# Kernel tuning notes

Hardware: AMD Instinct MI355X
Metric: run time of the kernel (lower is better)

Reference implementation:

```python
import jax, jax.numpy as jnp
import numpy as np

jax.config.update("jax_enable_x64", True)  # torch code casts to double for the logdet

B, N = 64, 512
MIN_LEN = 384  # variable sentence lengths to exercise padding path


def _matrix_tree_logZ(s_arc, mask):
    """log partition of non-projective trees via Kirchhoff's Matrix-Tree theorem.

    s_arc: [B, n, n] float32 scores of (dependent i, head j) pairs.
    mask:  [B, n] bool, column 0 is the root pseudo-word (False on input).
    """
    n = s_arc.shape[-1]
    m = mask.at[:, 0].set(True)                      # index_fill(1, 0, 1)
    chart = m[:, :, None] & m[:, None, :]            # [B, n, n]
    s = jnp.where(chart, s_arc, -jnp.inf)            # masked_fill(~chart, -inf)
    A = jnp.exp(s).astype(jnp.float64)               # exp(-inf) = 0 on padding
    d = A.sum(-1)                                    # D diagonal: row sums [B, n]
    eye = jnp.eye(n, dtype=A.dtype)
    L_full = d[:, :, None] * eye - A                 # D - A (Laplacian)
    # rows of padding tokens are identity rows (masked_scatter_ onto eye)
    L = jnp.where(m[:, :, None], L_full, eye[None])
    # logdet of the minor removing root row/col
    _, logabsdet = jnp.linalg.slogdet(L[:, 1:, 1:])
    return logabsdet.sum().astype(jnp.float32)


def setup_inputs() -> dict:
    key = jax.random.key(0)
    k1, k2, k3 = jax.random.split(key, 3)
    scores = jax.random.normal(k1, (B, N, N), dtype=jnp.float32)
    lens = jax.random.randint(k2, (B,), MIN_LEN, N)
    pos = jnp.arange(N)
    # first column False (root pseudo-word), True for real tokens < length
    mask = (pos[None, :] < lens[:, None]) & (pos[None, :] > 0)
    target = jax.random.randint(k3, (B, N), 0, N)    # gold head indices
    return {"scores": scores, "mask": mask, "target": target}


def reference(scores, mask, target):
    # forward(scores, mask, target, mbr=True, partial=False)
    logZ, marginals = jax.value_and_grad(_matrix_tree_logZ)(scores, mask)
    gold = jnp.take_along_axis(scores, target[..., None], axis=-1).squeeze(-1)  # [B, N]
    gold_score = jnp.where(mask, gold, 0.0).sum()    # scores[mask].sum()
    loss = (logZ - gold_score) / mask.sum()
    return loss, marginals
```

## Files before the change

kernel.cpp:

```cpp
#include <hip/hip_runtime.h>
#include <math.h>

#define BATCH 64
#define NN 512
#define MS 511
#define LDM 512
#define MSTRIDE ((size_t)MS*LDM)
#define OSTRIDE ((size_t)NN*NN)
#define PB 64
#define YW(r,c) (((r)<<5) + ((((c) + ((((r)>>3)&7)<<2))) & 31))

__global__ void k_convert(const void* __restrict__ mask_raw,
                          const void* __restrict__ tgt_raw,
                          int* __restrict__ cmask, int* __restrict__ ctgt) {
  int b = blockIdx.x;
  const unsigned char* mb = (const unsigned char*)mask_raw;
  const int* mw = (const int*)mask_raw;
  const int* tw = (const int*)tgt_raw;
  bool m_bytes = (mb[1] | mb[2] | mb[3]) != 0;
  bool m_64 = false;
  if (!m_bytes) {
    int acc = 0;
    for (int j = 1; j < 32; j += 2) acc |= mw[j];
    m_64 = (acc == 0);
  }
  int tacc = 0;
  for (int j = 1; j < 32; j += 2) tacc |= tw[j];
  bool t_64 = (tacc == 0);
  for (int i = threadIdx.x; i < NN; i += blockDim.x) {
    size_t idx = (size_t)b * NN + i;
    int mv;
    if (m_bytes) mv = mb[idx] != 0;
    else if (m_64) mv = mw[2 * idx] != 0;
    else mv = mw[idx] != 0;
    cmask[idx] = mv;
    ctgt[idx] = t_64 ? tw[2 * idx] : tw[idx];
  }
}

__global__ void k_build_M(const float* __restrict__ scores,
                          const int* __restrict__ mask,
                          float* __restrict__ M) {
  int b = blockIdx.y;
  int ip = blockIdx.x;
  int i = ip + 1;
  const int* mrow = mask + (size_t)b * NN;
  float* Mrow = M + (size_t)b * MSTRIDE + (size_t)ip * LDM;
  int tid = threadIdx.x;
  if (!mrow[i]) {
    for (int jp = tid; jp < MS; jp += 256)
      Mrow[jp] = (jp == ip) ? 1.0f : 0.0f;
    if (tid == 0) Mrow[MS] = 0.0f;
    return;
  }
  const float* srow = scores + ((size_t)b * NN + i) * NN;
  double part = 0.0;
  for (int j = tid; j < NN; j += 256) {
    bool mj = (j == 0) || (mrow[j] != 0);
    float e = mj ? expf(srow[j]) : 0.0f;
    part += (double)e;
    if (j >= 1) Mrow[j - 1] = -e;
  }
  __shared__ double red[256];
  red[tid] = part;
  __syncthreads();
  for (int s = 128; s > 0; s >>= 1) {
    if (tid < s) red[tid] += red[tid + s];
    __syncthreads();
  }
  if (tid == (i & 255)) Mrow[ip] += (float)red[0];
  if (tid == 0) Mrow[MS] = 0.0f;
}

__global__ __launch_bounds__(512) void k_panel64(float* __restrict__ M, int kb,
                                                 double* __restrict__ ld2) {
  int b = blockIdx.x;
  float* Mb = M + (size_t)b * MSTRIDE;
  int tid = threadIdx.x;
  __shared__ float A[64 * 65];
  __shared__ float XU[64 * 66];
  __shared__ float XL[64 * 66];
  __shared__ double lg[64];

  for (int idx = tid; idx < 64 * 64; idx += 512) {
    int r = idx >> 6, c = idx & 63;
    int gr = kb + r, gc = kb + c;
    A[r * 65 + c] = (gr < MS && gc < MS) ? Mb[(size_t)gr * LDM + gc]
                                         : ((r == c) ? 1.0f : 0.0f);
  }
  __syncthreads();

  int rr = tid >> 3, sub = tid & 7;
  for (int j = 0; j < 63; ++j) {
    if (rr > j) {
      float piv = A[j * 65 + j];
      float l = A[rr * 65 + j] / piv;
      if (sub == 0) A[rr * 65 + j] = l;
      for (int c = j + 1 + sub; c < 64; c += 8)
        A[rr * 65 + c] -= l * A[j * 65 + c];
    }
    __syncthreads();
  }
  if (tid < 64) lg[tid] = log(fabs((double)A[tid * 65 + tid]));
  __syncthreads();
  if (tid == 0) {
    double a = 0.0;
    for (int j = 0; j < 64; ++j) a += lg[j];
    ld2[(kb >> 6) * BATCH + b] = a;
  }

  {
    int c = rr;
    if (sub == 0) XU[c * 66 + c] = 1.0f / A[c * 65 + c];
    for (int r2 = c - 1; r2 >= 0; --r2) {
      float s = 0.0f;
      for (int k = r2 + 1 + sub; k <= c; k += 8)
        s += A[r2 * 65 + k] * XU[c * 66 + k];
      s += __shfl_xor(s, 1, 8);
      s += __shfl_xor(s, 2, 8);
      s += __shfl_xor(s, 4, 8);
      if (sub == 0) XU[c * 66 + r2] = -s / A[r2 * 65 + r2];
    }
  }
  {
    int c = rr;
    if (sub == 0) XL[c * 66 + c] = 1.0f;
    for (int r2 = c + 1; r2 < 64; ++r2) {
      float s = 0.0f;
      for (int k = c + sub; k < r2; k += 8)
        s += A[r2 * 65 + k] * XL[c * 66 + k];
      s += __shfl_xor(s, 1, 8);
      s += __shfl_xor(s, 2, 8);
      s += __shfl_xor(s, 4, 8);
      if (sub == 0) XL[c * 66 + r2] = -s;
    }
  }
  __syncthreads();
  for (int idx = tid; idx < 4096; idx += 512) {
    int r = idx >> 6, c = idx & 63;
    int gr = kb + r, gc = kb + c;
    if (gr < MS && gc < MS)
      Mb[(size_t)gr * LDM + gc] = (r > c) ? XL[c * 66 + r] : XU[c * 66 + r];
  }
}

__global__ __launch_bounds__(256) void k_trsm(float* __restrict__ M, int kb) {
  int b = blockIdx.z;
  int t = blockIdx.x;
  int side = blockIdx.y;
  float* Mb = M + (size_t)b * MSTRIDE;
  __shared__ float Fs[64 * 65];
  __shared__ float As[64 * 65];
  int tid = threadIdx.x;
  int off = kb + 64 + t * 64;
  for (int idx = tid; idx < 4096; idx += 256) {
    int r = idx >> 6, c = idx & 63;
    int gr = kb + r, gc = kb + c;
    float v;
    if (gr < MS && gc < MS) {
      float d = Mb[(size_t)gr * LDM + gc];
      if (side == 0) v = (r > c) ? d : (r == c ? 1.0f : 0.0f);
      else           v = (r <= c) ? d : 0.0f;
    } else {
      v = (r == c) ? 1.0f : 0.0f;
    }
    Fs[r * 65 + c] = v;
  }
  for (int idx = tid; idx < 4096; idx += 256) {
    int r = idx >> 6, c = idx & 63;
    int gr, gc;
    if (side == 0) { gr = kb + r; gc = off + c; }
    else           { gr = off + r; gc = kb + c; }
    As[r * 65 + c] = (gr < MS && gc < MS) ? Mb[(size_t)gr * LDM + gc] : 0.0f;
  }
  __syncthreads();
  int tx = tid & 15, ty = tid >> 4;
  float acc[4][4];
#pragma unroll
  for (int i = 0; i < 4; ++i)
#pragma unroll
    for (int j = 0; j < 4; ++j) acc[i][j] = 0.0f;
  if (side == 0) {
#pragma unroll 4
    for (int k = 0; k < 64; ++k) {
      float av[4], bv[4];
#pragma unroll
      for (int i = 0; i < 4; ++i) av[i] = Fs[(ty * 4 + i) * 65 + k];
#pragma unroll
      for (int j = 0; j < 4; ++j) bv[j] = As[k * 65 + tx * 4 + j];
#pragma unroll
      for (int i = 0; i < 4; ++i)
#pragma unroll
        for (int j = 0; j < 4; ++j) acc[i][j] = fmaf(av[i], bv[j], acc[i][j]);
    }
  } else {
#pragma unroll 4
    for (int k = 0; k < 64; ++k) {
      float av[4], bv[4];
#pragma unroll
      for (int i = 0; i < 4; ++i) av[i] = As[(ty * 4 + i) * 65 + k];
#pragma unroll
      for (int j = 0; j < 4; ++j) bv[j] = Fs[k * 65 + tx * 4 + j];
#pragma unroll
      for (int i = 0; i < 4; ++i)
#pragma unroll
        for (int j = 0; j < 4; ++j) acc[i][j] = fmaf(av[i], bv[j], acc[i][j]);
    }
  }
  if (side == 0) {
    int gc = off + tx * 4;
    if (gc < MS) {
#pragma unroll
      for (int i = 0; i < 4; ++i) {
        int gr = kb + ty * 4 + i;
        *(float4*)&Mb[(size_t)gr * LDM + gc] =
            make_float4(acc[i][0], acc[i][1], acc[i][2], acc[i][3]);
      }
    }
  } else {
#pragma unroll
    for (int i = 0; i < 4; ++i) {
      int gr = off + ty * 4 + i;
      if (gr < MS)
        *(float4*)&Mb[(size_t)gr * LDM + kb + tx * 4] =
            make_float4(acc[i][0], acc[i][1], acc[i][2], acc[i][3]);
    }
  }
}

__global__ __launch_bounds__(256) void k_update_panel(float* __restrict__ M, int kb,
                                                      double* __restrict__ ld2) {
  int b = blockIdx.z;
  float* Mb = M + (size_t)b * MSTRIDE;
  int row0 = kb + PB + blockIdx.x * 128;
  int col0 = kb + PB + blockIdx.y * 128;
  __shared__ __align__(16) float smem[128 * 68 + 64 * 132];
  __shared__ double lg[64];
  float* As = smem;
  float* Bs = smem + 128 * 68;
  int tid = threadIdx.x;
  for (int idx = tid; idx < 2048; idx += 256) {
    int r = idx >> 4, q = (idx & 15) * 4;
    int gr = row0 + r;
    float4 v = make_float4(0.f, 0.f, 0.f, 0.f);
    if (gr < MS) v = *(const float4*)&Mb[(size_t)gr * LDM + kb + q];
    *(float4*)&As[r * 68 + q] = v;
  }
  for (int idx = tid; idx < 2048; idx += 256) {
    int r = idx >> 5, q = (idx & 31) * 4;
    int gc = col0 + q;
    float4 v = make_float4(0.f, 0.f, 0.f, 0.f);
    if (gc < MS)
      v = *(const float4*)&Mb[(size_t)(kb + r) * LDM + gc];
    *(float4*)&Bs[r * 132 + q] = v;
  }
  __syncthreads();
  int tx = tid & 15, ty = tid >> 4;
  int gc0 = col0 + tx * 4, gc1 = gc0 + 64;
  bool c0v = gc0 < MS, c1v = gc1 < MS;
  float4 acc[8][2];
#pragma unroll
  for (int i = 0; i < 8; ++i) {
    int gr = row0 + ty + 16 * i;
    bool rv = gr < MS;
    acc[i][0] = (rv && c0v) ? *(const float4*)&Mb[(size_t)gr * LDM + gc0]
                            : make_float4(0.f, 0.f, 0.f, 0.f);
    acc[i][1] = (rv && c1v) ? *(const float4*)&Mb[(size_t)gr * LDM + gc1]
                            : make_float4(0.f, 0.f, 0.f, 0.f);
  }
#pragma unroll 2
  for (int k = 0; k < 64; ++k) {
    float4 b0 = *(const float4*)&Bs[k * 132 + tx * 4];
    float4 b1 = *(const float4*)&Bs[k * 132 + tx * 4 + 64];
    float av[8];
#pragma unroll
    for (int i = 0; i < 8; ++i) av[i] = As[(ty + 16 * i) * 68 + k];
#pragma unroll
    for (int i = 0; i < 8; ++i) {
      float a = av[i];
      acc[i][0].x = fmaf(-a, b0.x, acc[i][0].x);
      acc[i][0].y = fmaf(-a, b0.y, acc[i][0].y);
      acc[i][0].z = fmaf(-a, b0.z, acc[i][0].z);
      acc[i][0].w = fmaf(-a, b0.w, acc[i][0].w);
      acc[i][1].x = fmaf(-a, b1.x, acc[i][1].x);
      acc[i][1].y = fmaf(-a, b1.y, acc[i][1].y);
      acc[i][1].z = fmaf(-a, b1.z, acc[i][1].z);
      acc[i][1].w = fmaf(-a, b1.w, acc[i][1].w);
    }
  }
#pragma unroll
  for (int i = 0; i < 8; ++i) {
    int gr = row0 + ty + 16 * i;
    if (gr < MS) {
      if (c0v) *(float4*)&Mb[(size_t)gr * LDM + gc0] = acc[i][0];
      if (c1v) *(float4*)&Mb[(size_t)gr * LDM + gc1] = acc[i][1];
    }
  }

  if (blockIdx.x == 0 && blockIdx.y == 0) {
    int kbn = kb + PB;
    float* A2 = smem;
    float* XU = smem + 4160;
    float* XL = smem + 4160 + 4224;
    __syncthreads();
    for (int idx = tid; idx < 4096; idx += 256) {
      int r = idx >> 6, c = idx & 63;
      int gr = kbn + r, gc = kbn + c;
      A2[r * 65 + c] = (gr < MS && gc < MS) ? Mb[(size_t)gr * LDM + gc]
                                            : ((r == c) ? 1.0f : 0.0f);
    }
    __syncthreads();
    int rr = tid >> 2, sub = tid & 3;
    for (int j = 0; j < 63; ++j) {
      if (rr > j) {
        float piv = A2[j * 65 + j];
        float l = A2[rr * 65 + j] / piv;
        if (sub == 0) A2[rr * 65 + j] = l;
        for (int c = j + 1 + sub; c < 64; c += 4)
          A2[rr * 65 + c] -= l * A2[j * 65 + c];
      }
      __syncthreads();
    }
    if (tid < 64) lg[tid] = log(fabs((double)A2[tid * 65 + tid]));
    __syncthreads();
    if (tid == 0) {
      double a = 0.0;
      for (int j = 0; j < 64; ++j) a += lg[j];
      ld2[(kbn >> 6) * BATCH + b] = a;
    }
    {
      int c = rr;
      if (sub == 0) XU[c * 66 + c] = 1.0f / A2[c * 65 + c];
      for (int r2 = c - 1; r2 >= 0; --r2) {
        float s = 0.0f;
        for (int k = r2 + 1 + sub; k <= c; k += 4)
          s += A2[r2 * 65 + k] * XU[c * 66 + k];
        s += __shfl_xor(s, 1, 4);
        s += __shfl_xor(s, 2, 4);
        if (sub == 0) XU[c * 66 + r2] = -s / A2[r2 * 65 + r2];
      }
    }
    {
      int c = rr;
      if (sub == 0) XL[c * 66 + c] = 1.0f;
      for (int r2 = c + 1; r2 < 64; ++r2) {
        float s = 0.0f;
        for (int k = c + sub; k < r2; k += 4)
          s += A2[r2 * 65 + k] * XL[c * 66 + k];
        s += __shfl_xor(s, 1, 4);
        s += __shfl_xor(s, 2, 4);
        if (sub == 0) XL[c * 66 + r2] = -s;
      }
    }
    __syncthreads();
    for (int idx = tid; idx < 4096; idx += 256) {
      int r = idx >> 6, c = idx & 63;
      int gr = kbn + r, gc = kbn + c;
      if (gr < MS && gc < MS)
        Mb[(size_t)gr * LDM + gc] = (r > c) ? XL[c * 66 + r] : XU[c * 66 + r];
    }
  }
}

__device__ __forceinline__ void diag_pass(const float* __restrict__ Mb,
                                          float* __restrict__ Yt,
                                          int jb, int tid, int UPPER) {
  int drg = tid >> 3, dcg = tid & 7;
  int dr = jb + drg;
  bool vr = dr < MS;
  const float* Pr = Mb + (size_t)dr * LDM + jb;
  float4 da = make_float4(0.f, 0.f, 0.f, 0.f);
#pragma unroll 4
  for (int q = 0; q < 16; ++q) {
    float4 t = vr ? *(const float4*)&Pr[4 * q] : make_float4(0.f, 0.f, 0.f, 0.f);
#pragma unroll
    for (int m = 0; m < 4; ++m) {
      int cc = 4 * q + m;
      float tm = (m == 0) ? t.x : ((m == 1) ? t.y : ((m == 2) ? t.z : t.w));
      float a;
      if (UPPER) a = (drg <= cc) ? tm : 0.0f;
      else       a = (drg > cc) ? tm : ((drg == cc) ? 1.0f : 0.0f);
      float4 bv = *(const float4*)&Yt[YW(jb + cc, 4 * dcg)];
      da.x = fmaf(a, bv.x, da.x); da.y = fmaf(a, bv.y, da.y);
      da.z = fmaf(a, bv.z, da.z); da.w = fmaf(a, bv.w, da.w);
    }
  }
  __syncthreads();
  *(float4*)&Yt[YW(jb + drg, 4 * dcg)] = da;
  __syncthreads();
}

__device__ __forceinline__ void offdiag_pass(const float* __restrict__ Mb,
                                             float* __restrict__ Yt,
                                             int jb, int rowBase, int nr,
                                             int tid, int cg, int rg) {
  if (nr <= 0) return;
  int row0 = rowBase + 8 * rg;
  int nv = nr - 8 * rg;
  if (nv <= 0) return;
  nv = nv > 8 ? 8 : nv;
  float4 a0[8];
#pragma unroll
  for (int i = 0; i < 8; ++i)
    a0[i] = (i < nv) ? *(const float4*)&Yt[YW(row0 + i, 4 * cg)]
                     : make_float4(0.f, 0.f, 0.f, 0.f);
  const float* Ar = Mb + (size_t)row0 * LDM + jb;
#pragma unroll 2
  for (int kh = 0; kh < 16; ++kh) {
    float4 pA[8];
#pragma unroll
    for (int i = 0; i < 8; ++i)
      pA[i] = (i < nv) ? *(const float4*)&Ar[(size_t)i * LDM + 4 * kh]
                       : make_float4(0.f, 0.f, 0.f, 0.f);
    __builtin_amdgcn_s_setprio(1);
#pragma unroll
    for (int k = 0; k < 4; ++k) {
      float4 bv = *(const float4*)&Yt[YW(jb + 4 * kh + k, 4 * cg)];
#define AK(i) ((k == 0) ? pA[i].x : ((k == 1) ? pA[i].y : ((k == 2) ? pA[i].z : pA[i].w)))
#define RF(i) { \
      float av_ = AK(i); \
      a0[i].x = fmaf(-av_, bv.x, a0[i].x); a0[i].y = fmaf(-av_, bv.y, a0[i].y); \
      a0[i].z = fmaf(-av_, bv.z, a0[i].z); a0[i].w = fmaf(-av_, bv.w, a0[i].w); }
      RF(0) RF(1) RF(2) RF(3) RF(4) RF(5) RF(6) RF(7)
#undef RF
#undef AK
    }
    __builtin_amdgcn_s_setprio(0);
  }
#pragma unroll
  for (int i = 0; i < 8; ++i) {
    if (i < nv)
      *(float4*)&Yt[YW(row0 + i, 4 * cg)] = a0[i];
  }
}

__global__ __launch_bounds__(512, 4) void k_solve(const float* __restrict__ M,
                                                  const float* __restrict__ scores,
                                                  const int* __restrict__ mask,
                                                  float* __restrict__ out1) {
  int id = blockIdx.x;
  int xcd = id & 7, k7 = id >> 3;
  int b = xcd + ((k7 >> 4) << 3);
  int cb = k7 & 15;
  const float* Mb = M + (size_t)b * MSTRIDE;
  int tid = threadIdx.x;
  int c0 = cb * 32, fb = c0 & ~63;
  __shared__ __align__(16) float Yt[512 * 32];
  int cg = tid & 7, rg = tid >> 3;

  for (int idx = tid; idx < 4096; idx += 512)
    ((float4*)Yt)[idx] = make_float4(0.f, 0.f, 0.f, 0.f);
  __syncthreads();
  {
    int coff = c0 - fb;
    int r2 = tid >> 3, q4 = (tid & 7) << 2;
    int gr = fb + r2;
    int c_ = coff + q4;
    float e0, e1, e2, e3;
    if (gr < MS) {
      float4 d = *(const float4*)&Mb[(size_t)gr * LDM + fb + c_];
      e0 = (r2 > c_) ? d.x : ((r2 == c_) ? 1.f : 0.f);
      e1 = (r2 > c_ + 1) ? d.y : ((r2 == c_ + 1) ? 1.f : 0.f);
      e2 = (r2 > c_ + 2) ? d.z : ((r2 == c_ + 2) ? 1.f : 0.f);
      e3 = (r2 > c_ + 3) ? d.w : ((r2 == c_ + 3) ? 1.f : 0.f);
    } else {
      e0 = (r2 == c_) ? 1.f : 0.f;
      e1 = (r2 == c_ + 1) ? 1.f : 0.f;
      e2 = (r2 == c_ + 2) ? 1.f : 0.f;
      e3 = (r2 == c_ + 3) ? 1.f : 0.f;
    }
    *(float4*)&Yt[YW(gr, q4)] = make_float4(e0, e1, e2, e3);
  }
  __syncthreads();

  for (int jb = fb; jb < MS; jb += 64) {
    if (jb > fb) {
      __syncthreads();
      diag_pass(Mb, Yt, jb, tid, 0);
    }
    offdiag_pass(Mb, Yt, jb, jb + 64, MS - (jb + 64), tid, cg, rg);
  }
  for (int jb = 448; jb >= 0; jb -= 64) {
    __syncthreads();
    diag_pass(Mb, Yt, jb, tid, 1);
    offdiag_pass(Mb, Yt, jb, 0, jb, tid, cg, rg);
  }
  __syncthreads();

  const int* mrow = mask + (size_t)b * NN;
  const float* sb = scores + (size_t)b * NN * NN;
  float* ob = out1 + (size_t)b * OSTRIDE;
  for (int c = 0; c < 32; ++c) {
    int cgl = c0 + c;
    if (cgl >= MS) break;
    int i = cgl + 1;
    float* orow = ob + (size_t)i * NN;
    if (mrow[i] == 0) {
      orow[tid] = 0.0f;
    } else {
      float kd = Yt[YW(i - 1, c)];
      int k = tid;
      bool mk = (k == 0) || (mrow[k] != 0);
      float v = 0.0f;
      if (mk) {
        float s2 = (k >= 1) ? Yt[YW(k - 1, c)] : 0.0f;
        v = expf(sb[(size_t)i * NN + k]) * (kd - s2);
      }
      orow[k] = v;
    }
  }
  if (cb == 0) ob[tid] = 0.0f;
}

__global__ void k_gold(const float* __restrict__ scores,
                       const int* __restrict__ mask,
                       const int* __restrict__ target,
                       double* __restrict__ goldb, int* __restrict__ cntb) {
  int b = blockIdx.x;
  const int* mrow = mask + (size_t)b * NN;
  const int* trow = target + (size_t)b * NN;
  double g = 0.0;
  int c = 0;
  for (int i = threadIdx.x; i < NN; i += blockDim.x) {
    if (mrow[i] != 0) {
      g += (double)scores[((size_t)b * NN + i) * NN + trow[i]];
      c++;
    }
  }
  __shared__ double gs[256];
  __shared__ int cs[256];
  gs[threadIdx.x] = g;
  cs[threadIdx.x] = c;
  __syncthreads();
  for (int s = 128; s > 0; s >>= 1) {
    if (threadIdx.x < s) {
      gs[threadIdx.x] += gs[threadIdx.x + s];
      cs[threadIdx.x] += cs[threadIdx.x + s];
    }
    __syncthreads();
  }
  if (threadIdx.x == 0) { goldb[b] = gs[0]; cntb[b] = cs[0]; }
}

__global__ void k_final(const double* __restrict__ ld2,
                        const double* __restrict__ goldb,
                        const int* __restrict__ cntb, float* __restrict__ out) {
  int tid = threadIdx.x;
  double lz = 0.0, g = 0.0;
  double cnt = 0.0;
  for (int s = tid; s < 8 * BATCH; s += 256) lz += ld2[s];
  if (tid < BATCH) { g = goldb[tid]; cnt = (double)cntb[tid]; }
  __shared__ double r0[256], r1[256], r2[256];
  r0[tid] = lz; r1[tid] = g; r2[tid] = cnt;
  __syncthreads();
  for (int s = 128; s > 0; s >>= 1) {
    if (tid < s) { r0[tid] += r0[tid + s]; r1[tid] += r1[tid + s]; r2[tid] += r2[tid + s]; }
    __syncthreads();
  }
  if (tid == 0) out[0] = (float)((r0[0] - r1[0]) / r2[0]);
}

extern "C" void kernel_launch(void* const* d_in, const int* in_sizes, int n_in,
                              void* d_out, int out_size, void* d_ws, size_t ws_size,
                              hipStream_t stream) {
  const float* scores = (const float*)d_in[0];
  const void* mask_raw = d_in[1];
  const void* tgt_raw = d_in[2];
  float* out = (float*)d_out;
  float* out1 = out + 1;

  float* Mbuf = (float*)d_ws;
  size_t moff = (MSTRIDE * BATCH * sizeof(float) + 255) & ~(size_t)255;
  double* ld2 = (double*)((char*)d_ws + moff);
  double* goldb = ld2 + 8 * BATCH;
  int* cntb = (int*)(goldb + BATCH);
  int* cmask = cntb + BATCH;
  int* ctgt = cmask + BATCH * NN;

  k_convert<<<BATCH, 256, 0, stream>>>(mask_raw, tgt_raw, cmask, ctgt);
  k_build_M<<<dim3(MS, BATCH), 256, 0, stream>>>(scores, cmask, Mbuf);

  k_panel64<<<BATCH, 512, 0, stream>>>(Mbuf, 0, ld2);
  for (int kb = 0; kb + PB < MS; kb += PB) {
    int rem2 = MS - kb - PB;
    int nt64 = (rem2 + 63) / 64;
    k_trsm<<<dim3(nt64, 2, BATCH), 256, 0, stream>>>(Mbuf, kb);
    int nt128 = (rem2 + 127) / 128;
    k_update_panel<<<dim3(nt128, nt128, BATCH), 256, 0, stream>>>(Mbuf, kb, ld2);
  }

  k_solve<<<dim3(1024), 512, 0, stream>>>(Mbuf, scores, cmask, out1);
  k_gold<<<BATCH, 256, 0, stream>>>(scores, cmask, ctgt, goldb, cntb);
  k_final<<<1, 256, 0, stream>>>(ld2, goldb, cntb, out);
}
```

Baseline: 1.370 ms.

## Factor next diagonal panel in a dedicated block concurrently with trailing update

The next 64x64 diagonal block's LU factorization and inversion, which used to run serially in block (0,0) after its GEMM tile, now runs in an extra column of blocks. That block computes its own Schur update of the diagonal tile before factoring it, so it runs alongside the other update tiles instead of extending the critical path of one block. The diagonal GEMM block skips writing that 64x64 region to avoid a race. This adds one block row per launch and duplicates a small amount of update work.

```diff
diff --git a/kernel.cpp b/kernel.cpp
--- a/kernel.cpp
+++ b/kernel.cpp
@@ -228,86 +228,57 @@
   }
 }
 
-__global__ __launch_bounds__(256) void k_update_panel(float* __restrict__ M, int kb,
-                                                      double* __restrict__ ld2) {
+__global__ __launch_bounds__(256) void k_update_fp(float* __restrict__ M, int kb,
+                                                   double* __restrict__ ld2) {
   int b = blockIdx.z;
   float* Mb = M + (size_t)b * MSTRIDE;
-  int row0 = kb + PB + blockIdx.x * 128;
-  int col0 = kb + PB + blockIdx.y * 128;
+  int tid = threadIdx.x;
   __shared__ __align__(16) float smem[128 * 68 + 64 * 132];
   __shared__ double lg[64];
-  float* As = smem;
-  float* Bs = smem + 128 * 68;
-  int tid = threadIdx.x;
-  for (int idx = tid; idx < 2048; idx += 256) {
-    int r = idx >> 4, q = (idx & 15) * 4;
-    int gr = row0 + r;
-    float4 v = make_float4(0.f, 0.f, 0.f, 0.f);
-    if (gr < MS) v = *(const float4*)&Mb[(size_t)gr * LDM + kb + q];
-    *(float4*)&As[r * 68 + q] = v;
-  }
-  for (int idx = tid; idx < 2048; idx += 256) {
-    int r = idx >> 5, q = (idx & 31) * 4;
-    int gc = col0 + q;
-    float4 v = make_float4(0.f, 0.f, 0.f, 0.f);
-    if (gc < MS)
-      v = *(const float4*)&Mb[(size_t)(kb + r) * LDM + gc];
-    *(float4*)&Bs[r * 132 + q] = v;
-  }
-  __syncthreads();
-  int tx = tid & 15, ty = tid >> 4;
-  int gc0 = col0 + tx * 4, gc1 = gc0 + 64;
-  bool c0v = gc0 < MS, c1v = gc1 < MS;
-  float4 acc[8][2];
-#pragma unroll
-  for (int i = 0; i < 8; ++i) {
-    int gr = row0 + ty + 16 * i;
-    bool rv = gr < MS;
-    acc[i][0] = (rv && c0v) ? *(const float4*)&Mb[(size_t)gr * LDM + gc0]
-                            : make_float4(0.f, 0.f, 0.f, 0.f);
-    acc[i][1] = (rv && c1v) ? *(const float4*)&Mb[(size_t)gr * LDM + gc1]
-                            : make_float4(0.f, 0.f, 0.f, 0.f);
-  }
-#pragma unroll 2
-  for (int k = 0; k < 64; ++k) {
-    float4 b0 = *(const float4*)&Bs[k * 132 + tx * 4];
-    float4 b1 = *(const float4*)&Bs[k * 132 + tx * 4 + 64];
-    float av[8];
-#pragma unroll
-    for (int i = 0; i < 8; ++i) av[i] = As[(ty + 16 * i) * 68 + k];
-#pragma unroll
-    for (int i = 0; i < 8; ++i) {
-      float a = av[i];
-      acc[i][0].x = fmaf(-a, b0.x, acc[i][0].x);
-      acc[i][0].y = fmaf(-a, b0.y, acc[i][0].y);
-      acc[i][0].z = fmaf(-a, b0.z, acc[i][0].z);
-      acc[i][0].w = fmaf(-a, b0.w, acc[i][0].w);
-      acc[i][1].x = fmaf(-a, b1.x, acc[i][1].x);
-      acc[i][1].y = fmaf(-a, b1.y, acc[i][1].y);
-      acc[i][1].z = fmaf(-a, b1.z, acc[i][1].z);
-      acc[i][1].w = fmaf(-a, b1.w, acc[i][1].w);
-    }
-  }
-#pragma unroll
-  for (int i = 0; i < 8; ++i) {
-    int gr = row0 + ty + 16 * i;
-    if (gr < MS) {
-      if (c0v) *(float4*)&Mb[(size_t)gr * LDM + gc0] = acc[i][0];
-      if (c1v) *(float4*)&Mb[(size_t)gr * LDM + gc1] = acc[i][1];
-    }
-  }
-
-  if (blockIdx.x == 0 && blockIdx.y == 0) {
+
+  if (blockIdx.y == gridDim.y - 1) {
+    if (blockIdx.x != 0) return;
     int kbn = kb + PB;
-    float* A2 = smem;
-    float* XU = smem + 4160;
-    float* XL = smem + 4160 + 4224;
-    __syncthreads();
+    float* U12s = smem;
+    float* A2   = smem + 4160;
+    float* XU   = smem + 8320;
+    float* XL   = smem + 12544;
     for (int idx = tid; idx < 4096; idx += 256) {
-      int r = idx >> 6, c = idx & 63;
-      int gr = kbn + r, gc = kbn + c;
-      A2[r * 65 + c] = (gr < MS && gc < MS) ? Mb[(size_t)gr * LDM + gc]
-                                            : ((r == c) ? 1.0f : 0.0f);
+      int k = idx >> 6, c = idx & 63;
+      int gc = kbn + c;
+      U12s[k * 65 + c] = (gc < MS) ? Mb[(size_t)(kb + k) * LDM + gc] : 0.0f;
+    }
+    __syncthreads();
+    {
+      int r = tid >> 2, c0 = (tid & 3) * 16;
+      int gr = kbn + r;
+      float acc16[16];
+      if (gr < MS) {
+#pragma unroll
+        for (int c = 0; c < 16; ++c) {
+          int gc = kbn + c0 + c;
+          acc16[c] = (gc < MS) ? Mb[(size_t)gr * LDM + gc]
+                               : ((r == c0 + c) ? 1.0f : 0.0f);
+        }
+        const float* L21r = Mb + (size_t)gr * LDM + kb;
+        for (int kq = 0; kq < 16; ++kq) {
+          float4 l4 = *(const float4*)&L21r[4 * kq];
+          float lv[4] = {l4.x, l4.y, l4.z, l4.w};
+#pragma unroll
+          for (int m = 0; m < 4; ++m) {
+            int k = 4 * kq + m;
+            float l = lv[m];
+#pragma unroll
+            for (int c = 0; c < 16; ++c)
+              acc16[c] = fmaf(-l, U12s[k * 65 + c0 + c], acc16[c]);
+          }
+        }
+      } else {
+#pragma unroll
+        for (int c = 0; c < 16; ++c) acc16[c] = (r == c0 + c) ? 1.0f : 0.0f;
+      }
+#pragma unroll
+      for (int c = 0; c < 16; ++c) A2[r * 65 + c0 + c] = acc16[c];
     }
     __syncthreads();
     int rr = tid >> 2, sub = tid & 3;
@@ -358,6 +329,70 @@
       int gr = kbn + r, gc = kbn + c;
       if (gr < MS && gc < MS)
         Mb[(size_t)gr * LDM + gc] = (r > c) ? XL[c * 66 + r] : XU[c * 66 + r];
+    }
+    return;
+  }
+
+  float* As = smem;
+  float* Bs = smem + 128 * 68;
+  int row0 = kb + PB + blockIdx.x * 128;
+  int col0 = kb + PB + blockIdx.y * 128;
+  bool diagBlk = (blockIdx.x == 0 && blockIdx.y == 0);
+  for (int idx = tid; idx < 2048; idx += 256) {
+    int r = idx >> 4, q = (idx & 15) * 4;
+    int gr = row0 + r;
+    float4 v = make_float4(0.f, 0.f, 0.f, 0.f);
+    if (gr < MS) v = *(const float4*)&Mb[(size_t)gr * LDM + kb + q];
+    *(float4*)&As[r * 68 + q] = v;
+  }
+  for (int idx = tid; idx < 2048; idx += 256) {
+    int r = idx >> 5, q = (idx & 31) * 4;
+    int gc = col0 + q;
+    float4 v = make_float4(0.f, 0.f, 0.f, 0.f);
+    if (gc < MS)
+      v = *(const float4*)&Mb[(size_t)(kb + r) * LDM + gc];
+    *(float4*)&Bs[r * 132 + q] = v;
+  }
+  __syncthreads();
+  int tx = tid & 15, ty = tid >> 4;
+  int gc0 = col0 + tx * 4, gc1 = gc0 + 64;
+  bool c0v = gc0 < MS, c1v = gc1 < MS;
+  float4 acc[8][2];
+#pragma unroll
+  for (int i = 0; i < 8; ++i) {
+    int gr = row0 + ty + 16 * i;
+    bool rv = gr < MS;
+    acc[i][0] = (rv && c0v) ? *(const float4*)&Mb[(size_t)gr * LDM + gc0]
+                            : make_float4(0.f, 0.f, 0.f, 0.f);
+    acc[i][1] = (rv && c1v) ? *(const float4*)&Mb[(size_t)gr * LDM + gc1]
+                            : make_float4(0.f, 0.f, 0.f, 0.f);
+  }
+#pragma unroll 2
+  for (int k = 0; k < 64; ++k) {
+    float4 b0 = *(const float4*)&Bs[k * 132 + tx * 4];
+    float4 b1 = *(const float4*)&Bs[k * 132 + tx * 4 + 64];
+    float av[8];
+#pragma unroll
+    for (int i = 0; i < 8; ++i) av[i] = As[(ty + 16 * i) * 68 + k];
+#pragma unroll
+    for (int i = 0; i < 8; ++i) {
+      float a = av[i];
+      acc[i][0].x = fmaf(-a, b0.x, acc[i][0].x);
+      acc[i][0].y = fmaf(-a, b0.y, acc[i][0].y);
+      acc[i][0].z = fmaf(-a, b0.z, acc[i][0].z);
+      acc[i][0].w = fmaf(-a, b0.w, acc[i][0].w);
+      acc[i][1].x = fmaf(-a, b1.x, acc[i][1].x);
+      acc[i][1].y = fmaf(-a, b1.y, acc[i][1].y);
+      acc[i][1].z = fmaf(-a, b1.z, acc[i][1].z);
+      acc[i][1].w = fmaf(-a, b1.w, acc[i][1].w);
+    }
+  }
+#pragma unroll
+  for (int i = 0; i < 8; ++i) {
+    int gr = row0 + ty + 16 * i;
+    if (gr < MS) {
+      if (c0v && !(diagBlk && i < 4)) *(float4*)&Mb[(size_t)gr * LDM + gc0] = acc[i][0];
+      if (c1v) *(float4*)&Mb[(size_t)gr * LDM + gc1] = acc[i][1];
     }
   }
 }
@@ -586,7 +621,7 @@
     int nt64 = (rem2 + 63) / 64;
     k_trsm<<<dim3(nt64, 2, BATCH), 256, 0, stream>>>(Mbuf, kb);
     int nt128 = (rem2 + 127) / 128;
-    k_update_panel<<<dim3(nt128, nt128, BATCH), 256, 0, stream>>>(Mbuf, kb, ld2);
+    k_update_fp<<<dim3(nt128, nt128 + 1, BATCH), 256, 0, stream>>>(Mbuf, kb, ld2);
   }
 
   k_solve<<<dim3(1024), 512, 0, stream>>>(Mbuf, scores, cmask, out1);
```

After: 1.331 ms. -2.8%, faster.
